# Kernel optimization log

Measured on AMD Instinct MI355X. Metric: run time of the kernel, lower is better.

## Reference

```python
import jax, jax.numpy as jnp
import numpy as np

N = 20000      # nodes
E = 320000     # edges (before self-loops)
G = 64         # graphs in batch
H = 4          # attention heads
C = 64         # channels per head
HID = H * C    # 256
IN = 128       # input feature dim
LAT = 64       # latent dim
NEG = 0.2      # LeakyReLU negative slope (PyG GATConv default)
BN_EPS = 1e-5
N_LAYERS = 3


def setup_inputs() -> dict:
    key = jax.random.key(0)
    ks = jax.random.split(key, 24)
    s = 0.1
    return dict(
        x=jax.random.normal(ks[0], (N, IN), jnp.float32),
        edge_index=jax.random.randint(ks[1], (2, E), 0, N, dtype=jnp.int32),
        batch=jnp.sort(jax.random.randint(ks[2], (N,), 0, G, dtype=jnp.int32)),
        W0=jax.random.normal(ks[3], (IN, HID), jnp.float32) * s,
        W_rest=jax.random.normal(ks[4], (N_LAYERS - 1, HID, HID), jnp.float32) * s,
        att_src=jax.random.normal(ks[5], (N_LAYERS, H, C), jnp.float32) * s,
        att_dst=jax.random.normal(ks[6], (N_LAYERS, H, C), jnp.float32) * s,
        bias_conv=jax.random.normal(ks[7], (N_LAYERS, HID), jnp.float32) * s,
        bn_gamma=jax.random.uniform(ks[8], (N_LAYERS, HID), jnp.float32) + 0.5,
        bn_beta=jax.random.normal(ks[9], (N_LAYERS, HID), jnp.float32) * s,
        bn_mean=jax.random.normal(ks[10], (N_LAYERS, HID), jnp.float32) * s,
        bn_var=jax.random.uniform(ks[11], (N_LAYERS, HID), jnp.float32) + 0.5,
        lbn_gamma=jax.random.uniform(ks[12], (HID,), jnp.float32) + 0.5,
        lbn_beta=jax.random.normal(ks[13], (HID,), jnp.float32) * s,
        lbn_mean=jax.random.normal(ks[14], (HID,), jnp.float32) * s,
        lbn_var=jax.random.uniform(ks[15], (HID,), jnp.float32) + 0.5,
        fc_W=jax.random.normal(ks[16], (HID, LAT), jnp.float32) * s,
        fc_b=jax.random.normal(ks[17], (LAT,), jnp.float32) * s,
    )


def _gat_layer(x, src, dst, W, a_src, a_dst, bias):
    # linear transform -> [N, H, C]
    xp = (x @ W).reshape(N, H, C)
    # per-node attention scalars [N, H]
    al_s = (xp * a_src).sum(-1)
    al_d = (xp * a_dst).sum(-1)
    # per-edge logit for edge j->i: leaky_relu(a_s[j] + a_d[i])
    e = jax.nn.leaky_relu(al_s[src] + al_d[dst], NEG)  # [E', H]
    # softmax over incoming edges of each target node
    emax = jax.ops.segment_max(e, dst, num_segments=N)  # [N, H]
    ex = jnp.exp(e - emax[dst])
    denom = jax.ops.segment_sum(ex, dst, num_segments=N)
    alpha = ex / (denom[dst] + 1e-16)
    # weighted scatter-add of source features
    msg = xp[src] * alpha[:, :, None]                    # [E', H, C]
    out = jax.ops.segment_sum(msg, dst, num_segments=N)  # [N, H, C]
    return out.reshape(N, HID) + bias


def _bn_eval(x, gamma, beta, mean, var):
    return (x - mean) * jax.lax.rsqrt(var + BN_EPS) * gamma + beta


def reference(x, edge_index, batch, W0, W_rest, att_src, att_dst, bias_conv,
              bn_gamma, bn_beta, bn_mean, bn_var,
              lbn_gamma, lbn_beta, lbn_mean, lbn_var, fc_W, fc_b):
    # PyG convention: edge_index[0]=source, edge_index[1]=target; GATConv adds self-loops
    loop = jnp.arange(N, dtype=edge_index.dtype)
    src = jnp.concatenate([edge_index[0], loop])
    dst = jnp.concatenate([edge_index[1], loop])
    h = x
    for i in range(N_LAYERS):
        W = W0 if i == 0 else W_rest[i - 1]
        h = _gat_layer(h, src, dst, W, att_src[i], att_dst[i], bias_conv[i])
        h = _bn_eval(h, bn_gamma[i], bn_beta[i], bn_mean[i], bn_var[i])
        h = jax.nn.relu(h)
        # dropout is identity in eval mode
    pooled = jax.ops.segment_sum(h, batch, num_segments=G)  # [G, HID]
    pooled = _bn_eval(pooled, lbn_gamma, lbn_beta, lbn_mean, lbn_var)
    return pooled @ fc_W + fc_b  # [G, LAT]
```

## Files before the change

kernel.cpp:

```cpp
#include <hip/hip_runtime.h>
#include <hip/hip_bf16.h>
#include <cmath>

#define NN   20000
#define NE   320000
#define EE   (NE + NN)
#define NG   64
#define NH   4
#define NC   64
#define HIDD 256
#define IND  128
#define LATD 64
#define NEGS 0.2f
#define BNEPS 1e-5f
#define MPAD 20096
#define PSPLIT 16
#define NB   ((NN + 255) / 256)

#define BM 128
#define BN 64
#define BK 64

typedef __attribute__((ext_vector_type(8))) short short8;
typedef __attribute__((ext_vector_type(4))) float f32x4;

__device__ inline int lower_bound_i(const int* __restrict__ b, int n, int key) {
    int lo = 0, hi = n;
    while (lo < hi) { int mid = (lo + hi) >> 1; if (b[mid] < key) lo = mid + 1; else hi = mid; }
    return lo;
}

__device__ inline float bf2f(unsigned short u) {
    return __uint_as_float(((unsigned int)u) << 16);
}

__global__ void k_zero(int* __restrict__ p, int n) {
    int i = blockIdx.x * blockDim.x + threadIdx.x;
    if (i < n) p[i] = 0;
}

__global__ void k_cast_x(const float* __restrict__ x, __hip_bfloat16* __restrict__ hbx) {
    int i = blockIdx.x * blockDim.x + threadIdx.x;
    if (i >= NN * IND / 4) return;
    float4 v = ((const float4*)x)[i];
    union { __hip_bfloat16 b[4]; ushort4 u; } cv;
    cv.b[0] = __float2bfloat16(v.x); cv.b[1] = __float2bfloat16(v.y);
    cv.b[2] = __float2bfloat16(v.z); cv.b[3] = __float2bfloat16(v.w);
    ((ushort4*)hbx)[i] = cv.u;
}

__global__ void k_cast_wt_all(const float* __restrict__ W0, const float* __restrict__ Wr,
                              __hip_bfloat16* __restrict__ Wt3) {
    int k = blockIdx.x;
    int l = blockIdx.y;
    int n = threadIdx.x;
    int K = (l == 0) ? IND : HIDD;
    if (k >= K) return;
    const float* W = (l == 0) ? W0 : (Wr + (size_t)(l - 1) * HIDD * HIDD);
    size_t off = (l == 0) ? 0 : ((size_t)HIDD * IND + (size_t)(l - 1) * HIDD * HIDD);
    Wt3[off + (size_t)n * K + k] = __float2bfloat16(W[(size_t)k * HIDD + n]);
}

__global__ void k_hist(const int* __restrict__ ei, int* __restrict__ deg) {
    int e = blockIdx.x * blockDim.x + threadIdx.x;
    if (e >= EE) return;
    int d = (e < NE) ? ei[NE + e] : (e - NE);
    atomicAdd(&deg[d], 1);
}

__global__ __launch_bounds__(256) void k_blocksum(const int* __restrict__ deg,
                                                  int* __restrict__ bsum) {
    __shared__ int s[256];
    int i = blockIdx.x * 256 + threadIdx.x;
    s[threadIdx.x] = (i < NN) ? deg[i] : 0;
    __syncthreads();
    for (int off = 128; off > 0; off >>= 1) {
        if (threadIdx.x < off) s[threadIdx.x] += s[threadIdx.x + off];
        __syncthreads();
    }
    if (threadIdx.x == 0) bsum[blockIdx.x] = s[0];
}

__global__ __launch_bounds__(128) void k_scanbs(const int* __restrict__ bsum,
                                                int* __restrict__ boff,
                                                int* __restrict__ row_ptr) {
    __shared__ int s[128];
    int tid = threadIdx.x;
    int v = (tid < NB) ? bsum[tid] : 0;
    s[tid] = v;
    __syncthreads();
    for (int off = 1; off < 128; off <<= 1) {
        int t = (tid >= off) ? s[tid - off] : 0;
        __syncthreads();
        s[tid] += t;
        __syncthreads();
    }
    if (tid < NB) boff[tid] = s[tid] - v;
    if (tid == NB - 1) row_ptr[NN] = s[tid];
}

__global__ __launch_bounds__(256) void k_scanapply(const int* __restrict__ deg,
                                                   const int* __restrict__ boff,
                                                   int* __restrict__ row_ptr,
                                                   int* __restrict__ cursor) {
    __shared__ int s[256];
    int i = blockIdx.x * 256 + threadIdx.x;
    int v = (i < NN) ? deg[i] : 0;
    s[threadIdx.x] = v;
    __syncthreads();
    for (int off = 1; off < 256; off <<= 1) {
        int t = (threadIdx.x >= off) ? s[threadIdx.x - off] : 0;
        __syncthreads();
        s[threadIdx.x] += t;
        __syncthreads();
    }
    if (i < NN) {
        int excl = boff[blockIdx.x] + s[threadIdx.x] - v;
        row_ptr[i] = excl; cursor[i] = excl;
    }
}

__global__ void k_csr_scatter(const int* __restrict__ ei, int* __restrict__ cursor,
                              int* __restrict__ col_idx, int* __restrict__ dst_srt) {
    int e = blockIdx.x * blockDim.x + threadIdx.x;
    if (e >= EE) return;
    int s, d;
    if (e < NE) { s = ei[e]; d = ei[NE + e]; } else { s = d = e - NE; }
    int pos = atomicAdd(&cursor[d], 1);
    col_idx[pos] = s;
    dst_srt[pos] = d;
}

__global__ __launch_bounds__(256) void k_gemm(const short* __restrict__ A,
                                              const short* __restrict__ Bt,
                                              int K, __hip_bfloat16* __restrict__ Cb) {
    __shared__ char As[BM * BK * 2];
    __shared__ char Bs[BN * BK * 2];
    int tid = threadIdx.x;
    int lane = tid & 63;
    int wid = tid >> 6;
    int wm = wid >> 1, wn = wid & 1;
    int bm0 = blockIdx.x * BM, bn0 = blockIdx.y * BN;
    int r16 = lane & 15, kg = lane >> 4;

    f32x4 acc[4][2];
    #pragma unroll
    for (int m = 0; m < 4; ++m)
        #pragma unroll
        for (int n = 0; n < 2; ++n) acc[m][n] = (f32x4){0.f, 0.f, 0.f, 0.f};

    for (int k0 = 0; k0 < K; k0 += BK) {
        __syncthreads();
        #pragma unroll
        for (int p = 0; p < 4; ++p) {
            int row = p * 32 + (tid >> 3);
            int cg  = tid & 7;
            uint4 v = *(const uint4*)(A + (size_t)(bm0 + row) * K + k0 + cg * 8);
            *(uint4*)(As + row * 128 + ((cg * 16) ^ ((row & 7) << 4))) = v;
        }
        #pragma unroll
        for (int p = 0; p < 2; ++p) {
            int row = p * 32 + (tid >> 3);
            int cg  = tid & 7;
            uint4 v = *(const uint4*)(Bt + (size_t)(bn0 + row) * K + k0 + cg * 8);
            *(uint4*)(Bs + row * 128 + ((cg * 16) ^ ((row & 7) << 4))) = v;
        }
        __syncthreads();
        #pragma unroll
        for (int kk = 0; kk < 2; ++kk) {
            short8 af[4], bfr[2];
            int kb = (kk * 32 + kg * 8) * 2;
            #pragma unroll
            for (int m = 0; m < 4; ++m) {
                int row = wm * 64 + m * 16 + r16;
                af[m] = *(const short8*)(As + row * 128 + (kb ^ ((row & 7) << 4)));
            }
            #pragma unroll
            for (int n = 0; n < 2; ++n) {
                int row = wn * 32 + n * 16 + r16;
                bfr[n] = *(const short8*)(Bs + row * 128 + (kb ^ ((row & 7) << 4)));
            }
            #pragma unroll
            for (int m = 0; m < 4; ++m)
                #pragma unroll
                for (int n = 0; n < 2; ++n)
                    acc[m][n] = __builtin_amdgcn_mfma_f32_16x16x32_bf16(af[m], bfr[n], acc[m][n], 0, 0, 0);
        }
    }
    #pragma unroll
    for (int m = 0; m < 4; ++m) {
        int row = bm0 + wm * 64 + m * 16 + kg * 4;
        #pragma unroll
        for (int n = 0; n < 2; ++n) {
            int col = bn0 + wn * 32 + n * 16 + r16;
            #pragma unroll
            for (int r = 0; r < 4; ++r)
                Cb[(size_t)(row + r) * HIDD + col] = __float2bfloat16(acc[m][n][r]);
        }
    }
}

__global__ __launch_bounds__(256) void k_att2(const __hip_bfloat16* __restrict__ xpb,
                                              const float* __restrict__ a_src,
                                              const float* __restrict__ a_dst,
                                              float* __restrict__ al_s,
                                              float* __restrict__ al_d) {
    int wid = threadIdx.x >> 6, lane = threadIdx.x & 63;
    int node = blockIdx.x * 4 + wid;
    if (node >= NN) return;
    int hh = lane >> 4, sub = lane & 15;
    ushort4 u = ((const ushort4*)(xpb + (size_t)node * HIDD))[lane];
    float4 v = {bf2f(u.x), bf2f(u.y), bf2f(u.z), bf2f(u.w)};
    float4 ws = ((const float4*)a_src)[lane];
    float4 wd = ((const float4*)a_dst)[lane];
    float s = v.x * ws.x + v.y * ws.y + v.z * ws.z + v.w * ws.w;
    float d = v.x * wd.x + v.y * wd.y + v.z * wd.z + v.w * wd.w;
    #pragma unroll
    for (int m = 1; m < 16; m <<= 1) {
        s += __shfl_xor(s, m, 64);
        d += __shfl_xor(d, m, 64);
    }
    if (sub == 0) {
        al_s[node * NH + hh] = s;
        al_d[node * NH + hh] = d;
    }
}

__global__ void k_edgew(const int* __restrict__ col_idx, const int* __restrict__ dst_srt,
                        const float* __restrict__ al_s, const float* __restrict__ al_d,
                        float* __restrict__ ew) {
    int e = blockIdx.x * blockDim.x + threadIdx.x;
    if (e >= EE) return;
    int s = col_idx[e], d = dst_srt[e];
    float4 as = ((const float4*)al_s)[s];
    float4 ad = ((const float4*)al_d)[d];
    float4 l;
    l.x = as.x + ad.x; l.x = l.x > 0.f ? l.x : NEGS * l.x;
    l.y = as.y + ad.y; l.y = l.y > 0.f ? l.y : NEGS * l.y;
    l.z = as.z + ad.z; l.z = l.z > 0.f ? l.z : NEGS * l.z;
    l.w = as.w + ad.w; l.w = l.w > 0.f ? l.w : NEGS * l.w;
    float4 w = {__expf(l.x), __expf(l.y), __expf(l.z), __expf(l.w)};
    ((float4*)ew)[e] = w;
}

#define EDGE_BODY(I) \
    { den##I += w##I; \
      acc##I.x = fmaf(w##I, bf2f(xv##I.x), acc##I.x); \
      acc##I.y = fmaf(w##I, bf2f(xv##I.y), acc##I.y); \
      acc##I.z = fmaf(w##I, bf2f(xv##I.z), acc##I.z); \
      acc##I.w = fmaf(w##I, bf2f(xv##I.w), acc##I.w); }

__global__ __launch_bounds__(256) void k_gat_agg(
        const int* __restrict__ row_ptr, const int* __restrict__ col_idx,
        const float* __restrict__ ew,
        const __hip_bfloat16* __restrict__ xpb,
        const float* __restrict__ bias, const float* __restrict__ bg,
        const float* __restrict__ bb, const float* __restrict__ bm,
        const float* __restrict__ bv,
        float* __restrict__ h, __hip_bfloat16* __restrict__ hb, int wmask) {
    int wid = threadIdx.x >> 6, lane = threadIdx.x & 63;
    int node = blockIdx.x * 4 + wid;
    if (node >= NN) return;
    int lo = row_ptr[node], hi = row_ptr[node + 1];
    int hsel = lane >> 4;

    float4 acc0 = {0,0,0,0}, acc1 = {0,0,0,0}, acc2 = {0,0,0,0}, acc3 = {0,0,0,0};
    float den0 = 0.f, den1 = 0.f, den2 = 0.f, den3 = 0.f;

    int e = lo;
    for (; e + 3 < hi; e += 4) {
        int sc0 = col_idx[e], sc1 = col_idx[e + 1], sc2 = col_idx[e + 2], sc3 = col_idx[e + 3];
        float w0 = ew[(size_t)e * NH + hsel];
        float w1 = ew[(size_t)(e + 1) * NH + hsel];
        float w2 = ew[(size_t)(e + 2) * NH + hsel];
        float w3 = ew[(size_t)(e + 3) * NH + hsel];
        ushort4 xv0 = ((const ushort4*)(xpb + (size_t)sc0 * HIDD))[lane];
        ushort4 xv1 = ((const ushort4*)(xpb + (size_t)sc1 * HIDD))[lane];
        ushort4 xv2 = ((const ushort4*)(xpb + (size_t)sc2 * HIDD))[lane];
        ushort4 xv3 = ((const ushort4*)(xpb + (size_t)sc3 * HIDD))[lane];
        EDGE_BODY(0) EDGE_BODY(1) EDGE_BODY(2) EDGE_BODY(3)
    }
    for (; e < hi; ++e) {
        int sc0 = col_idx[e];
        float w0 = ew[(size_t)e * NH + hsel];
        ushort4 xv0 = ((const ushort4*)(xpb + (size_t)sc0 * HIDD))[lane];
        EDGE_BODY(0)
    }

    float den = (den0 + den1) + (den2 + den3);
    float inv = 1.f / (den + 1e-16f);
    float4 acc;
    acc.x = ((acc0.x + acc1.x) + (acc2.x + acc3.x)) * inv;
    acc.y = ((acc0.y + acc1.y) + (acc2.y + acc3.y)) * inv;
    acc.z = ((acc0.z + acc1.z) + (acc2.z + acc3.z)) * inv;
    acc.w = ((acc0.w + acc1.w) + (acc2.w + acc3.w)) * inv;

    float4 bi = ((const float4*)bias)[lane];
    float4 gg = ((const float4*)bg)[lane];
    float4 be = ((const float4*)bb)[lane];
    float4 mn = ((const float4*)bm)[lane];
    float4 vr = ((const float4*)bv)[lane];
    float4 val;
    val.x = (acc.x + bi.x - mn.x) * rsqrtf(vr.x + BNEPS) * gg.x + be.x;
    val.y = (acc.y + bi.y - mn.y) * rsqrtf(vr.y + BNEPS) * gg.y + be.y;
    val.z = (acc.z + bi.z - mn.z) * rsqrtf(vr.z + BNEPS) * gg.z + be.z;
    val.w = (acc.w + bi.w - mn.w) * rsqrtf(vr.w + BNEPS) * gg.w + be.w;
    val.x = val.x > 0.f ? val.x : 0.f;
    val.y = val.y > 0.f ? val.y : 0.f;
    val.z = val.z > 0.f ? val.z : 0.f;
    val.w = val.w > 0.f ? val.w : 0.f;
    if (wmask & 1)
        ((float4*)h)[(size_t)node * 64 + lane] = val;
    if (wmask & 2) {
        union { __hip_bfloat16 b[4]; ushort4 u; } cv;
        cv.b[0] = __float2bfloat16(val.x); cv.b[1] = __float2bfloat16(val.y);
        cv.b[2] = __float2bfloat16(val.z); cv.b[3] = __float2bfloat16(val.w);
        ((ushort4*)hb)[(size_t)node * 64 + lane] = cv.u;
    }
}

__global__ void k_pool2(const float* __restrict__ h, const int* __restrict__ batch,
                        float* __restrict__ partial) {
    int g = blockIdx.x, i = blockIdx.y, col = threadIdx.x;
    int lo = lower_bound_i(batch, NN, g);
    int hi = lower_bound_i(batch, NN, g + 1);
    int len = hi - lo;
    int a = lo + (int)((long)len * i / PSPLIT);
    int b = lo + (int)((long)len * (i + 1) / PSPLIT);
    float acc = 0.f;
    for (int n = a; n < b; ++n) acc += h[(size_t)n * HIDD + col];
    partial[((size_t)g * PSPLIT + i) * HIDD + col] = acc;
}

__global__ __launch_bounds__(64) void k_final(const float* __restrict__ partial,
                                              const float* __restrict__ lg,
                                              const float* __restrict__ lb,
                                              const float* __restrict__ lm,
                                              const float* __restrict__ lv,
                                              const float* __restrict__ fcW,
                                              const float* __restrict__ fcb,
                                              float* __restrict__ out) {
    __shared__ float ps[HIDD];
    int g = blockIdx.x, j = threadIdx.x;
    for (int k = j; k < HIDD; k += 64) {
        float s = 0.f;
        for (int i = 0; i < PSPLIT; ++i)
            s += partial[((size_t)g * PSPLIT + i) * HIDD + k];
        ps[k] = (s - lm[k]) * rsqrtf(lv[k] + BNEPS) * lg[k] + lb[k];
    }
    __syncthreads();
    float acc = 0.f;
    for (int k = 0; k < HIDD; ++k)
        acc = fmaf(ps[k], fcW[k * LATD + j], acc);
    out[g * LATD + j] = acc + fcb[j];
}

extern "C" void kernel_launch(void* const* d_in, const int* in_sizes, int n_in,
                              void* d_out, int out_size, void* d_ws, size_t ws_size,
                              hipStream_t stream) {
    const float* x     = (const float*)d_in[0];
    const int*   ei    = (const int*)d_in[1];
    const int*   batch = (const int*)d_in[2];
    const float* W0    = (const float*)d_in[3];
    const float* Wr    = (const float*)d_in[4];
    const float* asrc  = (const float*)d_in[5];
    const float* adst  = (const float*)d_in[6];
    const float* bconv = (const float*)d_in[7];
    const float* bng   = (const float*)d_in[8];
    const float* bnb   = (const float*)d_in[9];
    const float* bnm   = (const float*)d_in[10];
    const float* bnv   = (const float*)d_in[11];
    const float* lg    = (const float*)d_in[12];
    const float* lb    = (const float*)d_in[13];
    const float* lm    = (const float*)d_in[14];
    const float* lv    = (const float*)d_in[15];
    const float* fcW   = (const float*)d_in[16];
    const float* fcb   = (const float*)d_in[17];
    float* out = (float*)d_out;

    char* w = (char*)d_ws;
    size_t off = 0;
    auto alloc = [&](size_t bytes) {
        char* p = w + off;
        off += (bytes + 255) / 256 * 256;
        return p;
    };
    float* hbuf  = (float*)alloc((size_t)NN * HIDD * 4);
    float* al_s  = (float*)alloc((size_t)NN * NH * 4);
    float* al_d  = (float*)alloc((size_t)NN * NH * 4);
    float* ewbuf = (float*)alloc((size_t)EE * NH * 4);
    float* partial = (float*)alloc((size_t)NG * PSPLIT * HIDD * 4);
    __hip_bfloat16* hbx = (__hip_bfloat16*)alloc((size_t)MPAD * IND * 2);
    __hip_bfloat16* hb2 = (__hip_bfloat16*)alloc((size_t)MPAD * HIDD * 2);
    __hip_bfloat16* xpb = (__hip_bfloat16*)alloc((size_t)MPAD * HIDD * 2);
    __hip_bfloat16* Wt3 = (__hip_bfloat16*)alloc(((size_t)HIDD * IND + 2 * (size_t)HIDD * HIDD) * 2);
    int* deg     = (int*)alloc((size_t)NN * 4);
    int* row_ptr = (int*)alloc((size_t)(NN + 1) * 4);
    int* cursor  = (int*)alloc((size_t)NN * 4);
    int* col_idx = (int*)alloc((size_t)EE * 4);
    int* dst_srt = (int*)alloc((size_t)EE * 4);
    int* bsum    = (int*)alloc((size_t)NB * 4);
    int* boff    = (int*)alloc((size_t)NB * 4);

    hipLaunchKernelGGL(k_zero, dim3(NB), dim3(256), 0, stream, deg, NN);
    hipLaunchKernelGGL(k_hist, dim3((EE + 255) / 256), dim3(256), 0, stream, ei, deg);
    hipLaunchKernelGGL(k_blocksum, dim3(NB), dim3(256), 0, stream, deg, bsum);
    hipLaunchKernelGGL(k_scanbs, dim3(1), dim3(128), 0, stream, bsum, boff, row_ptr);
    hipLaunchKernelGGL(k_scanapply, dim3(NB), dim3(256), 0, stream, deg, boff, row_ptr, cursor);
    hipLaunchKernelGGL(k_csr_scatter, dim3((EE + 255) / 256), dim3(256), 0, stream,
                       ei, cursor, col_idx, dst_srt);

    hipLaunchKernelGGL(k_cast_x, dim3((NN * IND / 4 + 255) / 256), dim3(256), 0, stream, x, hbx);
    hipLaunchKernelGGL(k_cast_wt_all, dim3(HIDD, 3), dim3(HIDD), 0, stream, W0, Wr, Wt3);

    const size_t wtoff[3] = {0, (size_t)HIDD * IND, (size_t)HIDD * IND + (size_t)HIDD * HIDD};

    for (int layer = 0; layer < 3; ++layer) {
        int K = (layer == 0) ? IND : HIDD;
        const __hip_bfloat16* Ab = (layer == 0) ? hbx : hb2;
        int wmask = (layer == 2) ? 1 : 2;

        hipLaunchKernelGGL(k_gemm, dim3(MPAD / BM, HIDD / BN), dim3(256), 0, stream,
                           (const short*)Ab, (const short*)(Wt3 + wtoff[layer]), K, xpb);
        hipLaunchKernelGGL(k_att2, dim3((NN + 3) / 4), dim3(256), 0, stream,
                           xpb, asrc + layer * NH * NC, adst + layer * NH * NC, al_s, al_d);
        hipLaunchKernelGGL(k_edgew, dim3((EE + 255) / 256), dim3(256), 0, stream,
                           col_idx, dst_srt, al_s, al_d, ewbuf);
        hipLaunchKernelGGL(k_gat_agg, dim3((NN + 3) / 4), dim3(256), 0, stream,
                           row_ptr, col_idx, ewbuf, xpb,
                           bconv + layer * HIDD, bng + layer * HIDD, bnb + layer * HIDD,
                           bnm + layer * HIDD, bnv + layer * HIDD, hbuf, hb2, wmask);
    }

    hipLaunchKernelGGL(k_pool2, dim3(NG, PSPLIT), dim3(HIDD), 0, stream, hbuf, batch, partial);
    hipLaunchKernelGGL(k_final, dim3(NG), dim3(LATD), 0, stream,
                       partial, lg, lb, lm, lv, fcW, fcb, out);
}
```

Measured before the change: 214.0 us.

## Store projected features head-major and split aggregation per head

The GEMM output is now stored head-major as [H][MPAD][64], so each head's feature block sits in its own contiguous plane. The aggregation kernel gets a second grid dimension over heads, and each wavefront processes four edges at once, one per 16-lane slot. Partial sums are combined with cross-slot shuffles before the epilogue. The aim is a smaller per-head gather footprint and more edge-level parallelism, at the cost of four times as many blocks, re-reading row_ptr, col_idx and the edge weights once per head, and uncoalesced strided GEMM stores.

```diff
diff --git a/kernel.cpp b/kernel.cpp
--- a/kernel.cpp
+++ b/kernel.cpp
@@ -193,9 +193,10 @@
         #pragma unroll
         for (int n = 0; n < 2; ++n) {
             int col = bn0 + wn * 32 + n * 16 + r16;
+            size_t base = (size_t)(col >> 6) * MPAD * 64 + (col & 63);
             #pragma unroll
             for (int r = 0; r < 4; ++r)
-                Cb[(size_t)(row + r) * HIDD + col] = __float2bfloat16(acc[m][n][r]);
+                Cb[base + (size_t)(row + r) * 64] = __float2bfloat16(acc[m][n][r]);
         }
     }
 }
@@ -209,7 +210,7 @@
     int node = blockIdx.x * 4 + wid;
     if (node >= NN) return;
     int hh = lane >> 4, sub = lane & 15;
-    ushort4 u = ((const ushort4*)(xpb + (size_t)node * HIDD))[lane];
+    ushort4 u = ((const ushort4*)(xpb + ((size_t)hh * MPAD + node) * 64))[sub];
     float4 v = {bf2f(u.x), bf2f(u.y), bf2f(u.z), bf2f(u.w)};
     float4 ws = ((const float4*)a_src)[lane];
     float4 wd = ((const float4*)a_dst)[lane];
@@ -260,46 +261,52 @@
         float* __restrict__ h, __hip_bfloat16* __restrict__ hb, int wmask) {
     int wid = threadIdx.x >> 6, lane = threadIdx.x & 63;
     int node = blockIdx.x * 4 + wid;
+    int hh = blockIdx.y;
     if (node >= NN) return;
     int lo = row_ptr[node], hi = row_ptr[node + 1];
-    int hsel = lane >> 4;
-
-    float4 acc0 = {0,0,0,0}, acc1 = {0,0,0,0}, acc2 = {0,0,0,0}, acc3 = {0,0,0,0};
-    float den0 = 0.f, den1 = 0.f, den2 = 0.f, den3 = 0.f;
-
-    int e = lo;
-    for (; e + 3 < hi; e += 4) {
-        int sc0 = col_idx[e], sc1 = col_idx[e + 1], sc2 = col_idx[e + 2], sc3 = col_idx[e + 3];
-        float w0 = ew[(size_t)e * NH + hsel];
-        float w1 = ew[(size_t)(e + 1) * NH + hsel];
-        float w2 = ew[(size_t)(e + 2) * NH + hsel];
-        float w3 = ew[(size_t)(e + 3) * NH + hsel];
-        ushort4 xv0 = ((const ushort4*)(xpb + (size_t)sc0 * HIDD))[lane];
-        ushort4 xv1 = ((const ushort4*)(xpb + (size_t)sc1 * HIDD))[lane];
-        ushort4 xv2 = ((const ushort4*)(xpb + (size_t)sc2 * HIDD))[lane];
-        ushort4 xv3 = ((const ushort4*)(xpb + (size_t)sc3 * HIDD))[lane];
-        EDGE_BODY(0) EDGE_BODY(1) EDGE_BODY(2) EDGE_BODY(3)
-    }
-    for (; e < hi; ++e) {
+    int slot = lane >> 4, c = lane & 15;
+    const __hip_bfloat16* xph = xpb + (size_t)hh * MPAD * 64;
+
+    float4 acc0 = {0,0,0,0}, acc1 = {0,0,0,0};
+    float den0 = 0.f, den1 = 0.f;
+
+    int e = lo + slot;
+    for (; e + 4 < hi; e += 8) {
+        int sc0 = col_idx[e], sc1 = col_idx[e + 4];
+        float w0 = ew[(size_t)e * NH + hh];
+        float w1 = ew[(size_t)(e + 4) * NH + hh];
+        ushort4 xv0 = ((const ushort4*)(xph + (size_t)sc0 * 64))[c];
+        ushort4 xv1 = ((const ushort4*)(xph + (size_t)sc1 * 64))[c];
+        EDGE_BODY(0) EDGE_BODY(1)
+    }
+    if (e < hi) {
         int sc0 = col_idx[e];
-        float w0 = ew[(size_t)e * NH + hsel];
-        ushort4 xv0 = ((const ushort4*)(xpb + (size_t)sc0 * HIDD))[lane];
+        float w0 = ew[(size_t)e * NH + hh];
+        ushort4 xv0 = ((const ushort4*)(xph + (size_t)sc0 * 64))[c];
         EDGE_BODY(0)
     }
 
-    float den = (den0 + den1) + (den2 + den3);
+    float4 acc = {acc0.x + acc1.x, acc0.y + acc1.y, acc0.z + acc1.z, acc0.w + acc1.w};
+    float den = den0 + den1;
+    #pragma unroll
+    for (int m = 16; m < 64; m <<= 1) {
+        acc.x += __shfl_xor(acc.x, m, 64);
+        acc.y += __shfl_xor(acc.y, m, 64);
+        acc.z += __shfl_xor(acc.z, m, 64);
+        acc.w += __shfl_xor(acc.w, m, 64);
+        den   += __shfl_xor(den,   m, 64);
+    }
+    if (slot != 0) return;
+
     float inv = 1.f / (den + 1e-16f);
-    float4 acc;
-    acc.x = ((acc0.x + acc1.x) + (acc2.x + acc3.x)) * inv;
-    acc.y = ((acc0.y + acc1.y) + (acc2.y + acc3.y)) * inv;
-    acc.z = ((acc0.z + acc1.z) + (acc2.z + acc3.z)) * inv;
-    acc.w = ((acc0.w + acc1.w) + (acc2.w + acc3.w)) * inv;
-
-    float4 bi = ((const float4*)bias)[lane];
-    float4 gg = ((const float4*)bg)[lane];
-    float4 be = ((const float4*)bb)[lane];
-    float4 mn = ((const float4*)bm)[lane];
-    float4 vr = ((const float4*)bv)[lane];
+    acc.x *= inv; acc.y *= inv; acc.z *= inv; acc.w *= inv;
+
+    int pi = hh * 16 + c;
+    float4 bi = ((const float4*)bias)[pi];
+    float4 gg = ((const float4*)bg)[pi];
+    float4 be = ((const float4*)bb)[pi];
+    float4 mn = ((const float4*)bm)[pi];
+    float4 vr = ((const float4*)bv)[pi];
     float4 val;
     val.x = (acc.x + bi.x - mn.x) * rsqrtf(vr.x + BNEPS) * gg.x + be.x;
     val.y = (acc.y + bi.y - mn.y) * rsqrtf(vr.y + BNEPS) * gg.y + be.y;
@@ -310,12 +317,12 @@
     val.z = val.z > 0.f ? val.z : 0.f;
     val.w = val.w > 0.f ? val.w : 0.f;
     if (wmask & 1)
-        ((float4*)h)[(size_t)node * 64 + lane] = val;
+        ((float4*)h)[(size_t)node * 64 + pi] = val;
     if (wmask & 2) {
         union { __hip_bfloat16 b[4]; ushort4 u; } cv;
         cv.b[0] = __float2bfloat16(val.x); cv.b[1] = __float2bfloat16(val.y);
         cv.b[2] = __float2bfloat16(val.z); cv.b[3] = __float2bfloat16(val.w);
-        ((ushort4*)hb)[(size_t)node * 64 + lane] = cv.u;
+        ((ushort4*)hb)[(size_t)node * 64 + pi] = cv.u;
     }
 }
 
@@ -392,7 +399,7 @@
     float* partial = (float*)alloc((size_t)NG * PSPLIT * HIDD * 4);
     __hip_bfloat16* hbx = (__hip_bfloat16*)alloc((size_t)MPAD * IND * 2);
     __hip_bfloat16* hb2 = (__hip_bfloat16*)alloc((size_t)MPAD * HIDD * 2);
-    __hip_bfloat16* xpb = (__hip_bfloat16*)alloc((size_t)MPAD * HIDD * 2);
+    __hip_bfloat16* xpb = (__hip_bfloat16*)alloc((size_t)NH * MPAD * 64 * 2);
     __hip_bfloat16* Wt3 = (__hip_bfloat16*)alloc(((size_t)HIDD * IND + 2 * (size_t)HIDD * HIDD) * 2);
     int* deg     = (int*)alloc((size_t)NN * 4);
     int* row_ptr = (int*)alloc((size_t)(NN + 1) * 4);
@@ -426,7 +433,7 @@
                            xpb, asrc + layer * NH * NC, adst + layer * NH * NC, al_s, al_d);
         hipLaunchKernelGGL(k_edgew, dim3((EE + 255) / 256), dim3(256), 0, stream,
                            col_idx, dst_srt, al_s, al_d, ewbuf);
-        hipLaunchKernelGGL(k_gat_agg, dim3((NN + 3) / 4), dim3(256), 0, stream,
+        hipLaunchKernelGGL(k_gat_agg, dim3((NN + 3) / 4, NH), dim3(256), 0, stream,
                            row_ptr, col_idx, ewbuf, xpb,
                            bconv + layer * HIDD, bng + layer * HIDD, bnb + layer * HIDD,
                            bnm + layer * HIDD, bnv + layer * HIDD, hbuf, hb2, wmask);
```

Result: slower. 262.4 us (+22.6%).

## Fuse attention scalars into GEMM epilogue and edge weights into aggregation

Applied to the files above, without the earlier changes.

Computes per-node attention dot products inside the GEMM epilogue from fp32 accumulators, using shuffles plus a shared-memory reduction across the two warp columns, which removes the separate k_att2 pass. The per-edge exp weights are now computed on the fly in the aggregation kernel from gathered al_s values, which removes k_edgew, the [E,4] weight buffer and the dst_srt array. This saves two launches per layer and significant global memory traffic. In exchange the aggregation kernel does an extra exp per edge and a gathered load from al_s, and the GEMM epilogue gains a sync and shuffle work.

```diff
diff --git a/kernel.cpp b/kernel.cpp
--- a/kernel.cpp
+++ b/kernel.cpp
@@ -30,6 +30,14 @@
     return lo;
 }
 
+__device__ inline float sel4(float4 v, int h) {
+    float r = v.x;
+    r = (h == 1) ? v.y : r;
+    r = (h == 2) ? v.z : r;
+    r = (h == 3) ? v.w : r;
+    return r;
+}
+
 __device__ inline float bf2f(unsigned short u) {
     return __uint_as_float(((unsigned int)u) << 16);
 }
@@ -121,21 +129,26 @@
 }
 
 __global__ void k_csr_scatter(const int* __restrict__ ei, int* __restrict__ cursor,
-                              int* __restrict__ col_idx, int* __restrict__ dst_srt) {
+                              int* __restrict__ col_idx) {
     int e = blockIdx.x * blockDim.x + threadIdx.x;
     if (e >= EE) return;
     int s, d;
     if (e < NE) { s = ei[e]; d = ei[NE + e]; } else { s = d = e - NE; }
     int pos = atomicAdd(&cursor[d], 1);
     col_idx[pos] = s;
-    dst_srt[pos] = d;
 }
 
 __global__ __launch_bounds__(256) void k_gemm(const short* __restrict__ A,
                                               const short* __restrict__ Bt,
-                                              int K, __hip_bfloat16* __restrict__ Cb) {
+                                              int K, __hip_bfloat16* __restrict__ Cb,
+                                              const float* __restrict__ a_src,
+                                              const float* __restrict__ a_dst,
+                                              float* __restrict__ al_s,
+                                              float* __restrict__ al_d) {
     __shared__ char As[BM * BK * 2];
     __shared__ char Bs[BN * BK * 2];
+    __shared__ float redS[2][BM];
+    __shared__ float redD[2][BM];
     int tid = threadIdx.x;
     int lane = tid & 63;
     int wid = tid >> 6;
@@ -187,6 +200,7 @@
                     acc[m][n] = __builtin_amdgcn_mfma_f32_16x16x32_bf16(af[m], bfr[n], acc[m][n], 0, 0, 0);
         }
     }
+
     #pragma unroll
     for (int m = 0; m < 4; ++m) {
         int row = bm0 + wm * 64 + m * 16 + kg * 4;
@@ -198,61 +212,49 @@
                 Cb[(size_t)(row + r) * HIDD + col] = __float2bfloat16(acc[m][n][r]);
         }
     }
-}
-
-__global__ __launch_bounds__(256) void k_att2(const __hip_bfloat16* __restrict__ xpb,
-                                              const float* __restrict__ a_src,
-                                              const float* __restrict__ a_dst,
-                                              float* __restrict__ al_s,
-                                              float* __restrict__ al_d) {
-    int wid = threadIdx.x >> 6, lane = threadIdx.x & 63;
-    int node = blockIdx.x * 4 + wid;
-    if (node >= NN) return;
-    int hh = lane >> 4, sub = lane & 15;
-    ushort4 u = ((const ushort4*)(xpb + (size_t)node * HIDD))[lane];
-    float4 v = {bf2f(u.x), bf2f(u.y), bf2f(u.z), bf2f(u.w)};
-    float4 ws = ((const float4*)a_src)[lane];
-    float4 wd = ((const float4*)a_dst)[lane];
-    float s = v.x * ws.x + v.y * ws.y + v.z * ws.z + v.w * ws.w;
-    float d = v.x * wd.x + v.y * wd.y + v.z * wd.z + v.w * wd.w;
+
+    int headbase = bn0;
+    float as0 = a_src[headbase + wn * 32 + r16];
+    float as1 = a_src[headbase + wn * 32 + 16 + r16];
+    float ad0 = a_dst[headbase + wn * 32 + r16];
+    float ad1 = a_dst[headbase + wn * 32 + 16 + r16];
     #pragma unroll
-    for (int m = 1; m < 16; m <<= 1) {
-        s += __shfl_xor(s, m, 64);
-        d += __shfl_xor(d, m, 64);
-    }
-    if (sub == 0) {
-        al_s[node * NH + hh] = s;
-        al_d[node * NH + hh] = d;
-    }
-}
-
-__global__ void k_edgew(const int* __restrict__ col_idx, const int* __restrict__ dst_srt,
-                        const float* __restrict__ al_s, const float* __restrict__ al_d,
-                        float* __restrict__ ew) {
-    int e = blockIdx.x * blockDim.x + threadIdx.x;
-    if (e >= EE) return;
-    int s = col_idx[e], d = dst_srt[e];
-    float4 as = ((const float4*)al_s)[s];
-    float4 ad = ((const float4*)al_d)[d];
-    float4 l;
-    l.x = as.x + ad.x; l.x = l.x > 0.f ? l.x : NEGS * l.x;
-    l.y = as.y + ad.y; l.y = l.y > 0.f ? l.y : NEGS * l.y;
-    l.z = as.z + ad.z; l.z = l.z > 0.f ? l.z : NEGS * l.z;
-    l.w = as.w + ad.w; l.w = l.w > 0.f ? l.w : NEGS * l.w;
-    float4 w = {__expf(l.x), __expf(l.y), __expf(l.z), __expf(l.w)};
-    ((float4*)ew)[e] = w;
+    for (int m = 0; m < 4; ++m) {
+        #pragma unroll
+        for (int r = 0; r < 4; ++r) {
+            float ps = as0 * acc[m][0][r] + as1 * acc[m][1][r];
+            float pd = ad0 * acc[m][0][r] + ad1 * acc[m][1][r];
+            #pragma unroll
+            for (int msk = 1; msk < 16; msk <<= 1) {
+                ps += __shfl_xor(ps, msk, 64);
+                pd += __shfl_xor(pd, msk, 64);
+            }
+            if (r16 == 0) {
+                int rl = wm * 64 + m * 16 + kg * 4 + r;
+                redS[wn][rl] = ps;
+                redD[wn][rl] = pd;
+            }
+        }
+    }
+    __syncthreads();
+    if (tid < BM) {
+        int node = bm0 + tid;
+        al_s[node * NH + blockIdx.y] = redS[0][tid] + redS[1][tid];
+        al_d[node * NH + blockIdx.y] = redD[0][tid] + redD[1][tid];
+    }
 }
 
 #define EDGE_BODY(I) \
-    { den##I += w##I; \
-      acc##I.x = fmaf(w##I, bf2f(xv##I.x), acc##I.x); \
-      acc##I.y = fmaf(w##I, bf2f(xv##I.y), acc##I.y); \
-      acc##I.z = fmaf(w##I, bf2f(xv##I.z), acc##I.z); \
-      acc##I.w = fmaf(w##I, bf2f(xv##I.w), acc##I.w); }
+    { float l = as##I + adh; l = l > 0.f ? l : NEGS * l; \
+      float wt = __expf(l); den##I += wt; \
+      acc##I.x = fmaf(wt, bf2f(xv##I.x), acc##I.x); \
+      acc##I.y = fmaf(wt, bf2f(xv##I.y), acc##I.y); \
+      acc##I.z = fmaf(wt, bf2f(xv##I.z), acc##I.z); \
+      acc##I.w = fmaf(wt, bf2f(xv##I.w), acc##I.w); }
 
 __global__ __launch_bounds__(256) void k_gat_agg(
         const int* __restrict__ row_ptr, const int* __restrict__ col_idx,
-        const float* __restrict__ ew,
+        const float* __restrict__ al_s, const float* __restrict__ al_d,
         const __hip_bfloat16* __restrict__ xpb,
         const float* __restrict__ bias, const float* __restrict__ bg,
         const float* __restrict__ bb, const float* __restrict__ bm,
@@ -263,6 +265,7 @@
     if (node >= NN) return;
     int lo = row_ptr[node], hi = row_ptr[node + 1];
     int hsel = lane >> 4;
+    float adh = sel4(((const float4*)al_d)[node], hsel);
 
     float4 acc0 = {0,0,0,0}, acc1 = {0,0,0,0}, acc2 = {0,0,0,0}, acc3 = {0,0,0,0};
     float den0 = 0.f, den1 = 0.f, den2 = 0.f, den3 = 0.f;
@@ -270,10 +273,10 @@
     int e = lo;
     for (; e + 3 < hi; e += 4) {
         int sc0 = col_idx[e], sc1 = col_idx[e + 1], sc2 = col_idx[e + 2], sc3 = col_idx[e + 3];
-        float w0 = ew[(size_t)e * NH + hsel];
-        float w1 = ew[(size_t)(e + 1) * NH + hsel];
-        float w2 = ew[(size_t)(e + 2) * NH + hsel];
-        float w3 = ew[(size_t)(e + 3) * NH + hsel];
+        float as0 = al_s[sc0 * NH + hsel];
+        float as1 = al_s[sc1 * NH + hsel];
+        float as2 = al_s[sc2 * NH + hsel];
+        float as3 = al_s[sc3 * NH + hsel];
         ushort4 xv0 = ((const ushort4*)(xpb + (size_t)sc0 * HIDD))[lane];
         ushort4 xv1 = ((const ushort4*)(xpb + (size_t)sc1 * HIDD))[lane];
         ushort4 xv2 = ((const ushort4*)(xpb + (size_t)sc2 * HIDD))[lane];
@@ -282,7 +285,7 @@
     }
     for (; e < hi; ++e) {
         int sc0 = col_idx[e];
-        float w0 = ew[(size_t)e * NH + hsel];
+        float as0 = al_s[sc0 * NH + hsel];
         ushort4 xv0 = ((const ushort4*)(xpb + (size_t)sc0 * HIDD))[lane];
         EDGE_BODY(0)
     }
@@ -386,9 +389,8 @@
         return p;
     };
     float* hbuf  = (float*)alloc((size_t)NN * HIDD * 4);
-    float* al_s  = (float*)alloc((size_t)NN * NH * 4);
-    float* al_d  = (float*)alloc((size_t)NN * NH * 4);
-    float* ewbuf = (float*)alloc((size_t)EE * NH * 4);
+    float* al_s  = (float*)alloc((size_t)MPAD * NH * 4);
+    float* al_d  = (float*)alloc((size_t)MPAD * NH * 4);
     float* partial = (float*)alloc((size_t)NG * PSPLIT * HIDD * 4);
     __hip_bfloat16* hbx = (__hip_bfloat16*)alloc((size_t)MPAD * IND * 2);
     __hip_bfloat16* hb2 = (__hip_bfloat16*)alloc((size_t)MPAD * HIDD * 2);
@@ -398,7 +400,6 @@
     int* row_ptr = (int*)alloc((size_t)(NN + 1) * 4);
     int* cursor  = (int*)alloc((size_t)NN * 4);
     int* col_idx = (int*)alloc((size_t)EE * 4);
-    int* dst_srt = (int*)alloc((size_t)EE * 4);
     int* bsum    = (int*)alloc((size_t)NB * 4);
     int* boff    = (int*)alloc((size_t)NB * 4);
 
@@ -408,7 +409,7 @@
     hipLaunchKernelGGL(k_scanbs, dim3(1), dim3(128), 0, stream, bsum, boff, row_ptr);
     hipLaunchKernelGGL(k_scanapply, dim3(NB), dim3(256), 0, stream, deg, boff, row_ptr, cursor);
     hipLaunchKernelGGL(k_csr_scatter, dim3((EE + 255) / 256), dim3(256), 0, stream,
-                       ei, cursor, col_idx, dst_srt);
+                       ei, cursor, col_idx);
 
     hipLaunchKernelGGL(k_cast_x, dim3((NN * IND / 4 + 255) / 256), dim3(256), 0, stream, x, hbx);
     hipLaunchKernelGGL(k_cast_wt_all, dim3(HIDD, 3), dim3(HIDD), 0, stream, W0, Wr, Wt3);
@@ -421,13 +422,10 @@
         int wmask = (layer == 2) ? 1 : 2;
 
         hipLaunchKernelGGL(k_gemm, dim3(MPAD / BM, HIDD / BN), dim3(256), 0, stream,
-                           (const short*)Ab, (const short*)(Wt3 + wtoff[layer]), K, xpb);
-        hipLaunchKernelGGL(k_att2, dim3((NN + 3) / 4), dim3(256), 0, stream,
-                           xpb, asrc + layer * NH * NC, adst + layer * NH * NC, al_s, al_d);
-        hipLaunchKernelGGL(k_edgew, dim3((EE + 255) / 256), dim3(256), 0, stream,
-                           col_idx, dst_srt, al_s, al_d, ewbuf);
+                           (const short*)Ab, (const short*)(Wt3 + wtoff[layer]), K, xpb,
+                           asrc + layer * NH * NC, adst + layer * NH * NC, al_s, al_d);
         hipLaunchKernelGGL(k_gat_agg, dim3((NN + 3) / 4), dim3(256), 0, stream,
-                           row_ptr, col_idx, ewbuf, xpb,
+                           row_ptr, col_idx, al_s, al_d, xpb,
                            bconv + layer * HIDD, bng + layer * HIDD, bnb + layer * HIDD,
                            bnm + layer * HIDD, bnv + layer * HIDD, hbuf, hb2, wmask);
     }
```

After: 208.0 us. 1.03x faster.
